# Optimization experiments

Measured on AMD Instinct MI355X. Metric: run time of the kernel, lower is better.

## Reference

```python
import jax, jax.numpy as jnp
import numpy as np

HEAD = 8

def setup_inputs() -> dict:
    key = jax.random.key(0)
    k1, k2 = jax.random.split(key)
    B, S, D = 4, 2048, 512
    x = jax.random.normal(k1, (B, S, D), dtype=jnp.float32)
    Wq = jax.random.normal(k2, (D, D), dtype=jnp.float32) * (1.0 / np.sqrt(D))
    return {"x": x, "Wq": Wq}


def reference(x, Wq):
    # Faithful to source: Q, K, V all use linear_q (bug preserved).
    B, S, D = x.shape
    hd = D // HEAD
    q = jnp.einsum('bsd,de->bse', x, Wq)
    # Q = K = V = q
    qh = q.reshape(B, S, HEAD, hd).transpose(0, 2, 1, 3)  # [B,H,S,hd]
    # scale by sqrt(head_dim): inputs.shape[-1] inside ScaleDotAttentionLayer
    scores = jnp.einsum('bhqd,bhkd->bhqk', qh, qh) / jnp.sqrt(jnp.float32(hd))
    weights = jax.nn.softmax(scores, axis=-1)
    ctx = jnp.einsum('bhqk,bhkd->bhqd', weights, qh)
    out = ctx.transpose(0, 2, 1, 3).reshape(B, S, D)
    return out
```

## Files before the change

### kernel.cpp

```cpp
#include <hip/hip_runtime.h>
#include <hip/hip_fp16.h>
#include <math.h>

#define SS 2048
#define DD 512
#define NH 8
#define HD 64

typedef __attribute__((ext_vector_type(8))) short frag_ab;
typedef __attribute__((ext_vector_type(4))) float frag_cd;

static __device__ inline unsigned int pack_h2(float x, float y) {
    __half2 t = __floats2half2_rn(x, y);
    return *(unsigned int*)&t;
}

__global__ __launch_bounds__(256, 4) void gemm_kernel(const float* __restrict__ x,
                                                      const float* __restrict__ w,
                                                      unsigned short* __restrict__ q) {
    __shared__ __align__(16) unsigned short Ah[2][64 * 72];
    __shared__ __align__(16) unsigned short Bt[2][64 * 72];
    const int tid = threadIdx.x;
    const int lane = tid & 63, wv = tid >> 6;
    const int a = lane & 15, g = lane >> 4;
    const int bm = blockIdx.x, bn = blockIdx.y;

    frag_cd acc[4] = {};
    const int asr = tid >> 4;
    const int ac4 = (tid & 15) * 4;
    const int bnn = (tid & 31) * 2;
    const int bkk = (tid >> 5) * 8;

    float4 av[4];
    float2 bv[8];
    #pragma unroll
    for (int p = 0; p < 4; ++p)
        av[p] = *(const float4*)(x + (size_t)(bm * 64 + asr + p * 16) * 512 + ac4);
    #pragma unroll
    for (int j = 0; j < 8; ++j)
        bv[j] = *(const float2*)(w + (size_t)(bkk + j) * 512 + bn * 64 + bnn);

    for (int it = 0; it < 8; ++it) {
        const int cur = it & 1;
        #pragma unroll
        for (int p = 0; p < 4; ++p) {
            uint2 hh = { pack_h2(av[p].x, av[p].y), pack_h2(av[p].z, av[p].w) };
            *(uint2*)&Ah[cur][(asr + p * 16) * 72 + ac4] = hh;
        }
        {
            unsigned int t0[4], t1[4];
            #pragma unroll
            for (int j = 0; j < 4; ++j) {
                t0[j] = pack_h2(bv[2 * j].x, bv[2 * j + 1].x);
                t1[j] = pack_h2(bv[2 * j].y, bv[2 * j + 1].y);
            }
            *(uint4*)&Bt[cur][bnn * 72 + bkk]       = *(uint4*)t0;
            *(uint4*)&Bt[cur][(bnn + 1) * 72 + bkk] = *(uint4*)t1;
        }
        __syncthreads();
        if (it < 7) {
            const int k0 = (it + 1) * 64;
            #pragma unroll
            for (int p = 0; p < 4; ++p)
                av[p] = *(const float4*)(x + (size_t)(bm * 64 + asr + p * 16) * 512 + k0 + ac4);
            #pragma unroll
            for (int j = 0; j < 8; ++j)
                bv[j] = *(const float2*)(w + (size_t)(k0 + bkk + j) * 512 + bn * 64 + bnn);
        }
        #pragma unroll
        for (int kh = 0; kh < 2; ++kh) {
            const frag_ab bf = *(const frag_ab*)&Bt[cur][(wv * 16 + a) * 72 + kh * 32 + g * 8];
            #pragma unroll
            for (int mt = 0; mt < 4; ++mt) {
                const frag_ab af = *(const frag_ab*)&Ah[cur][(mt * 16 + a) * 72 + kh * 32 + g * 8];
                acc[mt] = __builtin_amdgcn_mfma_f32_16x16x32_f16(af, bf, acc[mt], 0, 0, 0);
            }
        }
    }
    #pragma unroll
    for (int mt = 0; mt < 4; ++mt)
        #pragma unroll
        for (int r = 0; r < 4; ++r) {
            const int m = bm * 64 + mt * 16 + g * 4 + r;
            const int n = bn * 64 + wv * 16 + a;
            __half hv = __float2half_rn(acc[mt][r]);
            q[(size_t)m * 512 + n] = *(unsigned short*)&hv;
        }
}

__global__ __launch_bounds__(512, 4) void attn_kernel(const __half* __restrict__ qg,
                                                      float* __restrict__ out) {
    __shared__ __align__(16) unsigned short Kt[2][64 * 72];
    __shared__ __align__(16) unsigned short Vt[2][64 * 64];
    __shared__ __align__(16) unsigned short Pq[8][32 * 72];

    const int tid = threadIdx.x;
    const int lane = tid & 63, wv = tid >> 6;
    const int a = lane & 15, g = lane >> 4;
    const int a7 = a & 7;
    const int qq = wv & 3;
    const int kv = wv >> 2;
    const int bid = blockIdx.x;
    const int qt = bid & 15;
    const int h  = (bid >> 4) & 7;
    const int b  = bid >> 7;

    const unsigned short* qbh = (const unsigned short*)qg + (size_t)b * SS * DD + h * HD;
    const int qrow0 = qt * 128 + qq * 32;

    frag_ab qf[2][2];
    const __half2 qsc = __float2half2_rn(0.18033688011112042f);
    #pragma unroll
    for (int nt = 0; nt < 2; ++nt)
        #pragma unroll
        for (int kh = 0; kh < 2; ++kh) {
            frag_ab t = *(const frag_ab*)(qbh + (size_t)(qrow0 + nt * 16 + a) * DD + kh * 32 + g * 8);
            __half2* ph = (__half2*)&t;
            #pragma unroll
            for (int i = 0; i < 4; ++i) ph[i] = __hmul2(ph[i], qsc);
            qf[nt][kh] = t;
        }

    frag_cd oacc[4][2] = {};
    float lsum[2] = {0.f, 0.f};

    const int t8 = tid & 255;
    const int f0 = (t8 & 31) * 2;
    const int u8 = t8 >> 5;
    const int r0 = u8 * 8;
    const int keybase = (tid >> 8) * 1024;
    unsigned short* Ks = Kt[tid >> 8];
    unsigned short* Vs = Vt[tid >> 8];
    unsigned short* myP = Pq[wv];

    unsigned int d[8];
    #pragma unroll
    for (int k = 0; k < 8; ++k)
        d[k] = *(const unsigned int*)(qbh + (size_t)(keybase + r0 + k) * DD + f0);

    const unsigned short* Kc = Kt[kv];
    const unsigned short* Vc = Vt[kv];
    const float coff = -11.541560327111707f;

    for (int it = 0; it < 16; ++it) {
        __syncthreads();
        #pragma unroll
        for (int k = 0; k < 8; ++k)
            *(unsigned int*)&Ks[(r0 + k) * 72 + f0] = d[k];
        {
            unsigned int vlo[4], vhi[4];
            #pragma unroll
            for (int j = 0; j < 4; ++j) {
                vlo[j] = (d[2 * j] & 0xFFFFu) | (d[2 * j + 1] << 16);
                vhi[j] = (d[2 * j] >> 16)     | (d[2 * j + 1] & 0xFFFF0000u);
            }
            *(uint4*)&Vs[f0 * 64 + ((u8 ^ (f0 & 7)) << 3)]             = *(uint4*)vlo;
            *(uint4*)&Vs[(f0 + 1) * 64 + ((u8 ^ ((f0 + 1) & 7)) << 3)] = *(uint4*)vhi;
        }
        __syncthreads();

        if (it + 1 < 16) {
            const int kb = keybase + (it + 1) * 64;
            #pragma unroll
            for (int k = 0; k < 8; ++k)
                d[k] = *(const unsigned int*)(qbh + (size_t)(kb + r0 + k) * DD + f0);
        }

        #pragma unroll
        for (int kt = 0; kt < 4; ++kt) {
            const frag_ab ka0 = *(const frag_ab*)&Kc[(kt * 16 + a) * 72 + g * 8];
            const frag_ab ka1 = *(const frag_ab*)&Kc[(kt * 16 + a) * 72 + 32 + g * 8];
            #pragma unroll
            for (int nt = 0; nt < 2; ++nt) {
                frag_cd c = {coff, coff, coff, coff};
                c = __builtin_amdgcn_mfma_f32_16x16x32_f16(ka0, qf[nt][0], c, 0, 0, 0);
                c = __builtin_amdgcn_mfma_f32_16x16x32_f16(ka1, qf[nt][1], c, 0, 0, 0);
                const float p0 = __builtin_amdgcn_exp2f(c[0]);
                const float p1 = __builtin_amdgcn_exp2f(c[1]);
                const float p2 = __builtin_amdgcn_exp2f(c[2]);
                const float p3 = __builtin_amdgcn_exp2f(c[3]);
                lsum[nt] += (p0 + p1) + (p2 + p3);
                uint2 pw = { pack_h2(p0, p1), pack_h2(p2, p3) };
                *(uint2*)&myP[(nt * 16 + a) * 72 + kt * 16 + g * 4] = pw;
            }
        }
        #pragma unroll
        for (int kh = 0; kh < 2; ++kh) {
            frag_ab va[4], pb[2];
            #pragma unroll
            for (int ft = 0; ft < 4; ++ft)
                va[ft] = *(const frag_ab*)&Vc[(ft * 16 + a) * 64 + (((4 * kh + g) ^ a7) << 3)];
            #pragma unroll
            for (int nt = 0; nt < 2; ++nt)
                pb[nt] = *(const frag_ab*)&myP[(nt * 16 + a) * 72 + kh * 32 + g * 8];
            #pragma unroll
            for (int ft = 0; ft < 4; ++ft)
                #pragma unroll
                for (int nt = 0; nt < 2; ++nt)
                    oacc[ft][nt] = __builtin_amdgcn_mfma_f32_16x16x32_f16(va[ft], pb[nt], oacc[ft][nt], 0, 0, 0);
        }
    }

    #pragma unroll
    for (int nt = 0; nt < 2; ++nt) {
        lsum[nt] += __shfl_xor(lsum[nt], 16, 64);
        lsum[nt] += __shfl_xor(lsum[nt], 32, 64);
    }
    __syncthreads();
    float* Obuf = (float*)&Pq[0][0];
    float* Lbuf = (float*)&Kt[0][0];
    if (kv == 1) {
        #pragma unroll
        for (int ft = 0; ft < 4; ++ft)
            #pragma unroll
            for (int nt = 0; nt < 2; ++nt)
                #pragma unroll
                for (int r = 0; r < 4; ++r)
                    Obuf[qq * 2112 + (ft * 16 + g * 4 + r) * 33 + nt * 16 + a] = oacc[ft][nt][r];
        if (g == 0)
            #pragma unroll
            for (int nt = 0; nt < 2; ++nt)
                Lbuf[qq * 32 + nt * 16 + a] = lsum[nt];
    }
    __syncthreads();
    if (kv == 0) {
        #pragma unroll
        for (int nt = 0; nt < 2; ++nt) {
            const float inv = 1.f / (lsum[nt] + Lbuf[qq * 32 + nt * 16 + a]);
            float* op = out + ((size_t)b * SS + qrow0 + nt * 16 + a) * DD + h * HD;
            #pragma unroll
            for (int ft = 0; ft < 4; ++ft) {
                const int fb = ft * 16 + g * 4;
                float4 vv = {
                    (oacc[ft][nt][0] + Obuf[qq * 2112 + (fb + 0) * 33 + nt * 16 + a]) * inv,
                    (oacc[ft][nt][1] + Obuf[qq * 2112 + (fb + 1) * 33 + nt * 16 + a]) * inv,
                    (oacc[ft][nt][2] + Obuf[qq * 2112 + (fb + 2) * 33 + nt * 16 + a]) * inv,
                    (oacc[ft][nt][3] + Obuf[qq * 2112 + (fb + 3) * 33 + nt * 16 + a]) * inv };
                *(float4*)(op + fb) = vv;
            }
        }
    }
}

extern "C" void kernel_launch(void* const* d_in, const int* in_sizes, int n_in,
                              void* d_out, int out_size, void* d_ws, size_t ws_size,
                              hipStream_t stream) {
    const float* x  = (const float*)d_in[0];
    const float* wq = (const float*)d_in[1];
    float* out = (float*)d_out;
    unsigned short* q_h = (unsigned short*)d_ws;

    dim3 ggrid(128, 8);
    gemm_kernel<<<ggrid, 256, 0, stream>>>(x, wq, q_h);
    attn_kernel<<<512, 512, 0, stream>>>((const __half*)q_h, out);
}
```

Baseline: 127.9 us.

## Keep softmax probabilities in registers via lane shuffles and halve query tile per block

The attention kernel no longer stages the P matrix through shared memory. Cross-lane shuffles rearrange the exp'd score fragments from the QK^T MFMA output layout into the B-operand layout for the PV MFMA. Each wave now handles 16 query rows instead of 32, the grid doubles to 1024 blocks, launch bounds request 8 blocks per SM, and the V swizzle is changed to match. This removes the LDS round trip and shrinks shared memory so occupancy can rise, at the cost of loading K/V tiles twice as often per query row and extra shuffle instructions.

```diff
diff --git a/kernel.cpp b/kernel.cpp
--- a/kernel.cpp
+++ b/kernel.cpp
@@ -88,41 +88,37 @@
         }
 }
 
-__global__ __launch_bounds__(512, 4) void attn_kernel(const __half* __restrict__ qg,
+__global__ __launch_bounds__(512, 8) void attn_kernel(const __half* __restrict__ qg,
                                                       float* __restrict__ out) {
     __shared__ __align__(16) unsigned short Kt[2][64 * 72];
     __shared__ __align__(16) unsigned short Vt[2][64 * 64];
-    __shared__ __align__(16) unsigned short Pq[8][32 * 72];
 
     const int tid = threadIdx.x;
     const int lane = tid & 63, wv = tid >> 6;
     const int a = lane & 15, g = lane >> 4;
-    const int a7 = a & 7;
     const int qq = wv & 3;
     const int kv = wv >> 2;
     const int bid = blockIdx.x;
-    const int qt = bid & 15;
-    const int h  = (bid >> 4) & 7;
-    const int b  = bid >> 7;
+    const int qt = bid & 31;
+    const int h  = (bid >> 5) & 7;
+    const int b  = bid >> 8;
 
     const unsigned short* qbh = (const unsigned short*)qg + (size_t)b * SS * DD + h * HD;
-    const int qrow0 = qt * 128 + qq * 32;
-
-    frag_ab qf[2][2];
+    const int qrow0 = qt * 64 + qq * 16;
+
+    frag_ab qf[2];
     const __half2 qsc = __float2half2_rn(0.18033688011112042f);
     #pragma unroll
-    for (int nt = 0; nt < 2; ++nt)
-        #pragma unroll
-        for (int kh = 0; kh < 2; ++kh) {
-            frag_ab t = *(const frag_ab*)(qbh + (size_t)(qrow0 + nt * 16 + a) * DD + kh * 32 + g * 8);
-            __half2* ph = (__half2*)&t;
-            #pragma unroll
-            for (int i = 0; i < 4; ++i) ph[i] = __hmul2(ph[i], qsc);
-            qf[nt][kh] = t;
-        }
-
-    frag_cd oacc[4][2] = {};
-    float lsum[2] = {0.f, 0.f};
+    for (int kh = 0; kh < 2; ++kh) {
+        frag_ab t = *(const frag_ab*)(qbh + (size_t)(qrow0 + a) * DD + kh * 32 + g * 8);
+        __half2* phh = (__half2*)&t;
+        #pragma unroll
+        for (int i = 0; i < 4; ++i) phh[i] = __hmul2(phh[i], qsc);
+        qf[kh] = t;
+    }
+
+    frag_cd oacc[4] = {};
+    float lsum = 0.f;
 
     const int t8 = tid & 255;
     const int f0 = (t8 & 31) * 2;
@@ -131,7 +127,7 @@
     const int keybase = (tid >> 8) * 1024;
     unsigned short* Ks = Kt[tid >> 8];
     unsigned short* Vs = Vt[tid >> 8];
-    unsigned short* myP = Pq[wv];
+    const int vsw = (u8 ^ (t8 & 7)) << 3;
 
     unsigned int d[8];
     #pragma unroll
@@ -141,6 +137,8 @@
     const unsigned short* Kc = Kt[kv];
     const unsigned short* Vc = Vt[kv];
     const float coff = -11.541560327111707f;
+    const bool hi32 = (lane & 32) != 0;
+    const bool hi16 = (lane & 16) != 0;
 
     for (int it = 0; it < 16; ++it) {
         __syncthreads();
@@ -154,8 +152,8 @@
                 vlo[j] = (d[2 * j] & 0xFFFFu) | (d[2 * j + 1] << 16);
                 vhi[j] = (d[2 * j] >> 16)     | (d[2 * j + 1] & 0xFFFF0000u);
             }
-            *(uint4*)&Vs[f0 * 64 + ((u8 ^ (f0 & 7)) << 3)]             = *(uint4*)vlo;
-            *(uint4*)&Vs[(f0 + 1) * 64 + ((u8 ^ ((f0 + 1) & 7)) << 3)] = *(uint4*)vhi;
+            *(uint4*)&Vs[f0 * 64 + vsw]       = *(uint4*)vlo;
+            *(uint4*)&Vs[(f0 + 1) * 64 + vsw] = *(uint4*)vhi;
         }
         __syncthreads();
 
@@ -166,78 +164,84 @@
                 d[k] = *(const unsigned int*)(qbh + (size_t)(kb + r0 + k) * DD + f0);
         }
 
+        unsigned int ph[4][2];
         #pragma unroll
         for (int kt = 0; kt < 4; ++kt) {
             const frag_ab ka0 = *(const frag_ab*)&Kc[(kt * 16 + a) * 72 + g * 8];
             const frag_ab ka1 = *(const frag_ab*)&Kc[(kt * 16 + a) * 72 + 32 + g * 8];
-            #pragma unroll
-            for (int nt = 0; nt < 2; ++nt) {
-                frag_cd c = {coff, coff, coff, coff};
-                c = __builtin_amdgcn_mfma_f32_16x16x32_f16(ka0, qf[nt][0], c, 0, 0, 0);
-                c = __builtin_amdgcn_mfma_f32_16x16x32_f16(ka1, qf[nt][1], c, 0, 0, 0);
-                const float p0 = __builtin_amdgcn_exp2f(c[0]);
-                const float p1 = __builtin_amdgcn_exp2f(c[1]);
-                const float p2 = __builtin_amdgcn_exp2f(c[2]);
-                const float p3 = __builtin_amdgcn_exp2f(c[3]);
-                lsum[nt] += (p0 + p1) + (p2 + p3);
-                uint2 pw = { pack_h2(p0, p1), pack_h2(p2, p3) };
-                *(uint2*)&myP[(nt * 16 + a) * 72 + kt * 16 + g * 4] = pw;
-            }
+            frag_cd c = {coff, coff, coff, coff};
+            c = __builtin_amdgcn_mfma_f32_16x16x32_f16(ka0, qf[0], c, 0, 0, 0);
+            c = __builtin_amdgcn_mfma_f32_16x16x32_f16(ka1, qf[1], c, 0, 0, 0);
+            const float p0 = __builtin_amdgcn_exp2f(c[0]);
+            const float p1 = __builtin_amdgcn_exp2f(c[1]);
+            const float p2 = __builtin_amdgcn_exp2f(c[2]);
+            const float p3 = __builtin_amdgcn_exp2f(c[3]);
+            lsum += (p0 + p1) + (p2 + p3);
+            ph[kt][0] = pack_h2(p0, p1);
+            ph[kt][1] = pack_h2(p2, p3);
+        }
+        #pragma unroll
+        for (int w = 0; w < 2; ++w) {
+            unsigned int s01 = hi32 ? ph[0][w] : ph[1][w];
+            unsigned int t01 = __shfl_xor(s01, 32, 64);
+            ph[0][w] = hi32 ? t01 : ph[0][w];
+            ph[1][w] = hi32 ? ph[1][w] : t01;
+            unsigned int s23 = hi32 ? ph[2][w] : ph[3][w];
+            unsigned int t23 = __shfl_xor(s23, 32, 64);
+            ph[2][w] = hi32 ? t23 : ph[2][w];
+            ph[3][w] = hi32 ? ph[3][w] : t23;
+        }
+        #pragma unroll
+        for (int w = 0; w < 2; ++w) {
+            unsigned int s01 = hi16 ? ph[0][w] : ph[1][w];
+            unsigned int t01 = __shfl_xor(s01, 16, 64);
+            ph[0][w] = hi16 ? t01 : ph[0][w];
+            ph[1][w] = hi16 ? ph[1][w] : t01;
+            unsigned int s23 = hi16 ? ph[2][w] : ph[3][w];
+            unsigned int t23 = __shfl_xor(s23, 16, 64);
+            ph[2][w] = hi16 ? t23 : ph[2][w];
+            ph[3][w] = hi16 ? ph[3][w] : t23;
         }
         #pragma unroll
         for (int kh = 0; kh < 2; ++kh) {
-            frag_ab va[4], pb[2];
-            #pragma unroll
-            for (int ft = 0; ft < 4; ++ft)
-                va[ft] = *(const frag_ab*)&Vc[(ft * 16 + a) * 64 + (((4 * kh + g) ^ a7) << 3)];
-            #pragma unroll
-            for (int nt = 0; nt < 2; ++nt)
-                pb[nt] = *(const frag_ab*)&myP[(nt * 16 + a) * 72 + kh * 32 + g * 8];
-            #pragma unroll
-            for (int ft = 0; ft < 4; ++ft)
-                #pragma unroll
-                for (int nt = 0; nt < 2; ++nt)
-                    oacc[ft][nt] = __builtin_amdgcn_mfma_f32_16x16x32_f16(va[ft], pb[nt], oacc[ft][nt], 0, 0, 0);
-        }
-    }
-
-    #pragma unroll
-    for (int nt = 0; nt < 2; ++nt) {
-        lsum[nt] += __shfl_xor(lsum[nt], 16, 64);
-        lsum[nt] += __shfl_xor(lsum[nt], 32, 64);
-    }
+            __attribute__((aligned(16))) unsigned int pw4[4] =
+                { ph[2 * kh][0], ph[2 * kh][1], ph[2 * kh + 1][0], ph[2 * kh + 1][1] };
+            const frag_ab pb = *(const frag_ab*)pw4;
+            #pragma unroll
+            for (int ft = 0; ft < 4; ++ft) {
+                const frag_ab va = *(const frag_ab*)
+                    &Vc[(ft * 16 + a) * 64 + (((4 * kh + g) ^ ((a >> 1) & 7)) << 3)];
+                oacc[ft] = __builtin_amdgcn_mfma_f32_16x16x32_f16(va, pb, oacc[ft], 0, 0, 0);
+            }
+        }
+    }
+
+    lsum += __shfl_xor(lsum, 16, 64);
+    lsum += __shfl_xor(lsum, 32, 64);
     __syncthreads();
-    float* Obuf = (float*)&Pq[0][0];
-    float* Lbuf = (float*)&Kt[0][0];
+    float* Obuf = (float*)&Kt[0][0];
+    float* Lbuf = (float*)&Vt[0][0];
     if (kv == 1) {
         #pragma unroll
         for (int ft = 0; ft < 4; ++ft)
             #pragma unroll
-            for (int nt = 0; nt < 2; ++nt)
-                #pragma unroll
-                for (int r = 0; r < 4; ++r)
-                    Obuf[qq * 2112 + (ft * 16 + g * 4 + r) * 33 + nt * 16 + a] = oacc[ft][nt][r];
-        if (g == 0)
-            #pragma unroll
-            for (int nt = 0; nt < 2; ++nt)
-                Lbuf[qq * 32 + nt * 16 + a] = lsum[nt];
+            for (int r = 0; r < 4; ++r)
+                Obuf[qq * 1088 + (ft * 16 + g * 4 + r) * 17 + a] = oacc[ft][r];
+        if (g == 0) Lbuf[qq * 16 + a] = lsum;
     }
     __syncthreads();
     if (kv == 0) {
-        #pragma unroll
-        for (int nt = 0; nt < 2; ++nt) {
-            const float inv = 1.f / (lsum[nt] + Lbuf[qq * 32 + nt * 16 + a]);
-            float* op = out + ((size_t)b * SS + qrow0 + nt * 16 + a) * DD + h * HD;
-            #pragma unroll
-            for (int ft = 0; ft < 4; ++ft) {
-                const int fb = ft * 16 + g * 4;
-                float4 vv = {
-                    (oacc[ft][nt][0] + Obuf[qq * 2112 + (fb + 0) * 33 + nt * 16 + a]) * inv,
-                    (oacc[ft][nt][1] + Obuf[qq * 2112 + (fb + 1) * 33 + nt * 16 + a]) * inv,
-                    (oacc[ft][nt][2] + Obuf[qq * 2112 + (fb + 2) * 33 + nt * 16 + a]) * inv,
-                    (oacc[ft][nt][3] + Obuf[qq * 2112 + (fb + 3) * 33 + nt * 16 + a]) * inv };
-                *(float4*)(op + fb) = vv;
-            }
+        const float inv = 1.f / (lsum + Lbuf[qq * 16 + a]);
+        float* op = out + ((size_t)b * SS + qrow0 + a) * DD + h * HD;
+        #pragma unroll
+        for (int ft = 0; ft < 4; ++ft) {
+            const int fb = ft * 16 + g * 4;
+            float4 vv = {
+                (oacc[ft][0] + Obuf[qq * 1088 + (fb + 0) * 17 + a]) * inv,
+                (oacc[ft][1] + Obuf[qq * 1088 + (fb + 1) * 17 + a]) * inv,
+                (oacc[ft][2] + Obuf[qq * 1088 + (fb + 2) * 17 + a]) * inv,
+                (oacc[ft][3] + Obuf[qq * 1088 + (fb + 3) * 17 + a]) * inv };
+            *(float4*)(op + fb) = vv;
         }
     }
 }
@@ -252,5 +256,5 @@
 
     dim3 ggrid(128, 8);
     gemm_kernel<<<ggrid, 256, 0, stream>>>(x, wq, q_h);
-    attn_kernel<<<512, 512, 0, stream>>>((const __half*)q_h, out);
-}
+    attn_kernel<<<1024, 512, 0, stream>>>((const __half*)q_h, out);
+}
```

Result: slower. 144.1 us (+12.7%).

## Keep softmax probabilities in registers via lane shuffles instead of LDS round-trip

Applied to the files above, without the earlier changes.

Removes the per-wave P staging buffer in shared memory. The fp16-packed probabilities are now transposed between MFMA output and input layouts with two stages of cross-lane xor shuffles, and the V swizzle pattern is changed to match. Shared memory is collapsed into one byte array, which lowers LDS use per block and may allow more blocks per CU. The cost is extra shuffle and select instructions and more register pressure in the inner loop.

```diff
diff --git a/kernel.cpp b/kernel.cpp
--- a/kernel.cpp
+++ b/kernel.cpp
@@ -90,14 +90,13 @@
 
 __global__ __launch_bounds__(512, 4) void attn_kernel(const __half* __restrict__ qg,
                                                       float* __restrict__ out) {
-    __shared__ __align__(16) unsigned short Kt[2][64 * 72];
-    __shared__ __align__(16) unsigned short Vt[2][64 * 64];
-    __shared__ __align__(16) unsigned short Pq[8][32 * 72];
+    __shared__ __align__(16) unsigned char LDSB[34816];
+    unsigned short* KtB = (unsigned short*)LDSB;
+    unsigned short* VtB = (unsigned short*)(LDSB + 18432);
 
     const int tid = threadIdx.x;
     const int lane = tid & 63, wv = tid >> 6;
     const int a = lane & 15, g = lane >> 4;
-    const int a7 = a & 7;
     const int qq = wv & 3;
     const int kv = wv >> 2;
     const int bid = blockIdx.x;
@@ -115,9 +114,9 @@
         #pragma unroll
         for (int kh = 0; kh < 2; ++kh) {
             frag_ab t = *(const frag_ab*)(qbh + (size_t)(qrow0 + nt * 16 + a) * DD + kh * 32 + g * 8);
-            __half2* ph = (__half2*)&t;
-            #pragma unroll
-            for (int i = 0; i < 4; ++i) ph[i] = __hmul2(ph[i], qsc);
+            __half2* phh = (__half2*)&t;
+            #pragma unroll
+            for (int i = 0; i < 4; ++i) phh[i] = __hmul2(phh[i], qsc);
             qf[nt][kh] = t;
         }
 
@@ -129,18 +128,20 @@
     const int u8 = t8 >> 5;
     const int r0 = u8 * 8;
     const int keybase = (tid >> 8) * 1024;
-    unsigned short* Ks = Kt[tid >> 8];
-    unsigned short* Vs = Vt[tid >> 8];
-    unsigned short* myP = Pq[wv];
+    unsigned short* Ks = KtB + (tid >> 8) * 4608;
+    unsigned short* Vs = VtB + (tid >> 8) * 4096;
+    const int vsw = (u8 ^ (t8 & 7)) << 3;
 
     unsigned int d[8];
     #pragma unroll
     for (int k = 0; k < 8; ++k)
         d[k] = *(const unsigned int*)(qbh + (size_t)(keybase + r0 + k) * DD + f0);
 
-    const unsigned short* Kc = Kt[kv];
-    const unsigned short* Vc = Vt[kv];
+    const unsigned short* Kc = KtB + kv * 4608;
+    const unsigned short* Vc = VtB + kv * 4096;
     const float coff = -11.541560327111707f;
+    const bool hi32 = (lane & 32) != 0;
+    const bool hi16 = (lane & 16) != 0;
 
     for (int it = 0; it < 16; ++it) {
         __syncthreads();
@@ -154,8 +155,8 @@
                 vlo[j] = (d[2 * j] & 0xFFFFu) | (d[2 * j + 1] << 16);
                 vhi[j] = (d[2 * j] >> 16)     | (d[2 * j + 1] & 0xFFFF0000u);
             }
-            *(uint4*)&Vs[f0 * 64 + ((u8 ^ (f0 & 7)) << 3)]             = *(uint4*)vlo;
-            *(uint4*)&Vs[(f0 + 1) * 64 + ((u8 ^ ((f0 + 1) & 7)) << 3)] = *(uint4*)vhi;
+            *(uint4*)&Vs[f0 * 64 + vsw]       = *(uint4*)vlo;
+            *(uint4*)&Vs[(f0 + 1) * 64 + vsw] = *(uint4*)vhi;
         }
         __syncthreads();
 
@@ -166,6 +167,7 @@
                 d[k] = *(const unsigned int*)(qbh + (size_t)(kb + r0 + k) * DD + f0);
         }
 
+        unsigned int ph[2][4][2];
         #pragma unroll
         for (int kt = 0; kt < 4; ++kt) {
             const frag_ab ka0 = *(const frag_ab*)&Kc[(kt * 16 + a) * 72 + g * 8];
@@ -180,24 +182,52 @@
                 const float p2 = __builtin_amdgcn_exp2f(c[2]);
                 const float p3 = __builtin_amdgcn_exp2f(c[3]);
                 lsum[nt] += (p0 + p1) + (p2 + p3);
-                uint2 pw = { pack_h2(p0, p1), pack_h2(p2, p3) };
-                *(uint2*)&myP[(nt * 16 + a) * 72 + kt * 16 + g * 4] = pw;
+                ph[nt][kt][0] = pack_h2(p0, p1);
+                ph[nt][kt][1] = pack_h2(p2, p3);
+            }
+        }
+        #pragma unroll
+        for (int nt = 0; nt < 2; ++nt) {
+            #pragma unroll
+            for (int w = 0; w < 2; ++w) {
+                unsigned int s01 = hi32 ? ph[nt][0][w] : ph[nt][1][w];
+                unsigned int t01 = __shfl_xor(s01, 32, 64);
+                ph[nt][0][w] = hi32 ? t01 : ph[nt][0][w];
+                ph[nt][1][w] = hi32 ? ph[nt][1][w] : t01;
+                unsigned int s23 = hi32 ? ph[nt][2][w] : ph[nt][3][w];
+                unsigned int t23 = __shfl_xor(s23, 32, 64);
+                ph[nt][2][w] = hi32 ? t23 : ph[nt][2][w];
+                ph[nt][3][w] = hi32 ? ph[nt][3][w] : t23;
+            }
+            #pragma unroll
+            for (int w = 0; w < 2; ++w) {
+                unsigned int s01 = hi16 ? ph[nt][0][w] : ph[nt][1][w];
+                unsigned int t01 = __shfl_xor(s01, 16, 64);
+                ph[nt][0][w] = hi16 ? t01 : ph[nt][0][w];
+                ph[nt][1][w] = hi16 ? ph[nt][1][w] : t01;
+                unsigned int s23 = hi16 ? ph[nt][2][w] : ph[nt][3][w];
+                unsigned int t23 = __shfl_xor(s23, 16, 64);
+                ph[nt][2][w] = hi16 ? t23 : ph[nt][2][w];
+                ph[nt][3][w] = hi16 ? ph[nt][3][w] : t23;
             }
         }
         #pragma unroll
         for (int kh = 0; kh < 2; ++kh) {
-            frag_ab va[4], pb[2];
+            frag_ab va[4];
             #pragma unroll
             for (int ft = 0; ft < 4; ++ft)
-                va[ft] = *(const frag_ab*)&Vc[(ft * 16 + a) * 64 + (((4 * kh + g) ^ a7) << 3)];
-            #pragma unroll
-            for (int nt = 0; nt < 2; ++nt)
-                pb[nt] = *(const frag_ab*)&myP[(nt * 16 + a) * 72 + kh * 32 + g * 8];
-            #pragma unroll
-            for (int ft = 0; ft < 4; ++ft)
+                va[ft] = *(const frag_ab*)
+                    &Vc[(ft * 16 + a) * 64 + (((4 * kh + g) ^ ((a >> 1) & 7)) << 3)];
+            #pragma unroll
+            for (int nt = 0; nt < 2; ++nt) {
+                __attribute__((aligned(16))) unsigned int pw4[4] =
+                    { ph[nt][2 * kh][0], ph[nt][2 * kh][1],
+                      ph[nt][2 * kh + 1][0], ph[nt][2 * kh + 1][1] };
+                const frag_ab pb = *(const frag_ab*)pw4;
                 #pragma unroll
-                for (int nt = 0; nt < 2; ++nt)
-                    oacc[ft][nt] = __builtin_amdgcn_mfma_f32_16x16x32_f16(va[ft], pb[nt], oacc[ft][nt], 0, 0, 0);
+                for (int ft = 0; ft < 4; ++ft)
+                    oacc[ft][nt] = __builtin_amdgcn_mfma_f32_16x16x32_f16(va[ft], pb, oacc[ft][nt], 0, 0, 0);
+            }
         }
     }
 
@@ -207,8 +237,8 @@
         lsum[nt] += __shfl_xor(lsum[nt], 32, 64);
     }
     __syncthreads();
-    float* Obuf = (float*)&Pq[0][0];
-    float* Lbuf = (float*)&Kt[0][0];
+    float* Obuf = (float*)LDSB;
+    float* Lbuf = (float*)(LDSB + 33792);
     if (kv == 1) {
         #pragma unroll
         for (int ft = 0; ft < 4; ++ft)
```

Result: no change. 128.6 us (+0.6%).

## Feed softmax probabilities to PV MFMA straight from registers, dropping P LDS staging

Applied to the files above, without the earlier changes.

Instead of writing the exp'd probabilities to a per-wave LDS buffer and reading them back as 16x16x32 operands, each QK^T output fragment is packed into fp16 registers and used directly as the B operand of 16x16x16 MFMAs against V. The V swizzle is changed to match the new 4-element read pattern, and LDS is consolidated into one shared byte array, shrinking it by removing the P buffer. This removes LDS round-trips and the associated latency for P, and may raise occupancy, at the cost of using twice as many smaller-K MFMA instructions for the PV product.

```diff
diff --git a/kernel.cpp b/kernel.cpp
--- a/kernel.cpp
+++ b/kernel.cpp
@@ -9,6 +9,7 @@
 
 typedef __attribute__((ext_vector_type(8))) short frag_ab;
 typedef __attribute__((ext_vector_type(4))) float frag_cd;
+typedef __attribute__((ext_vector_type(4))) _Float16 frag_b4;
 
 static __device__ inline unsigned int pack_h2(float x, float y) {
     __half2 t = __floats2half2_rn(x, y);
@@ -90,14 +91,13 @@
 
 __global__ __launch_bounds__(512, 4) void attn_kernel(const __half* __restrict__ qg,
                                                       float* __restrict__ out) {
-    __shared__ __align__(16) unsigned short Kt[2][64 * 72];
-    __shared__ __align__(16) unsigned short Vt[2][64 * 64];
-    __shared__ __align__(16) unsigned short Pq[8][32 * 72];
+    __shared__ __align__(16) unsigned char LDSB[34816];
+    unsigned short* KtB = (unsigned short*)LDSB;
+    unsigned short* VtB = (unsigned short*)(LDSB + 18432);
 
     const int tid = threadIdx.x;
     const int lane = tid & 63, wv = tid >> 6;
     const int a = lane & 15, g = lane >> 4;
-    const int a7 = a & 7;
     const int qq = wv & 3;
     const int kv = wv >> 2;
     const int bid = blockIdx.x;
@@ -115,9 +115,9 @@
         #pragma unroll
         for (int kh = 0; kh < 2; ++kh) {
             frag_ab t = *(const frag_ab*)(qbh + (size_t)(qrow0 + nt * 16 + a) * DD + kh * 32 + g * 8);
-            __half2* ph = (__half2*)&t;
-            #pragma unroll
-            for (int i = 0; i < 4; ++i) ph[i] = __hmul2(ph[i], qsc);
+            __half2* phh = (__half2*)&t;
+            #pragma unroll
+            for (int i = 0; i < 4; ++i) phh[i] = __hmul2(phh[i], qsc);
             qf[nt][kh] = t;
         }
 
@@ -129,18 +129,19 @@
     const int u8 = t8 >> 5;
     const int r0 = u8 * 8;
     const int keybase = (tid >> 8) * 1024;
-    unsigned short* Ks = Kt[tid >> 8];
-    unsigned short* Vs = Vt[tid >> 8];
-    unsigned short* myP = Pq[wv];
+    unsigned short* Ks = KtB + (tid >> 8) * 4608;
+    unsigned short* Vs = VtB + (tid >> 8) * 4096;
+    const int vsw = (u8 ^ (t8 & 7)) << 3;
 
     unsigned int d[8];
     #pragma unroll
     for (int k = 0; k < 8; ++k)
         d[k] = *(const unsigned int*)(qbh + (size_t)(keybase + r0 + k) * DD + f0);
 
-    const unsigned short* Kc = Kt[kv];
-    const unsigned short* Vc = Vt[kv];
+    const unsigned short* Kc = KtB + kv * 4608;
+    const unsigned short* Vc = VtB + kv * 4096;
     const float coff = -11.541560327111707f;
+    const int sv = (a >> 1) & 7;
 
     for (int it = 0; it < 16; ++it) {
         __syncthreads();
@@ -154,8 +155,8 @@
                 vlo[j] = (d[2 * j] & 0xFFFFu) | (d[2 * j + 1] << 16);
                 vhi[j] = (d[2 * j] >> 16)     | (d[2 * j + 1] & 0xFFFF0000u);
             }
-            *(uint4*)&Vs[f0 * 64 + ((u8 ^ (f0 & 7)) << 3)]             = *(uint4*)vlo;
-            *(uint4*)&Vs[(f0 + 1) * 64 + ((u8 ^ ((f0 + 1) & 7)) << 3)] = *(uint4*)vhi;
+            *(uint4*)&Vs[f0 * 64 + vsw]       = *(uint4*)vlo;
+            *(uint4*)&Vs[(f0 + 1) * 64 + vsw] = *(uint4*)vhi;
         }
         __syncthreads();
 
@@ -170,6 +171,7 @@
         for (int kt = 0; kt < 4; ++kt) {
             const frag_ab ka0 = *(const frag_ab*)&Kc[(kt * 16 + a) * 72 + g * 8];
             const frag_ab ka1 = *(const frag_ab*)&Kc[(kt * 16 + a) * 72 + 32 + g * 8];
+            frag_b4 pbk[2];
             #pragma unroll
             for (int nt = 0; nt < 2; ++nt) {
                 frag_cd c = {coff, coff, coff, coff};
@@ -180,24 +182,19 @@
                 const float p2 = __builtin_amdgcn_exp2f(c[2]);
                 const float p3 = __builtin_amdgcn_exp2f(c[3]);
                 lsum[nt] += (p0 + p1) + (p2 + p3);
-                uint2 pw = { pack_h2(p0, p1), pack_h2(p2, p3) };
-                *(uint2*)&myP[(nt * 16 + a) * 72 + kt * 16 + g * 4] = pw;
-            }
-        }
-        #pragma unroll
-        for (int kh = 0; kh < 2; ++kh) {
-            frag_ab va[4], pb[2];
-            #pragma unroll
-            for (int ft = 0; ft < 4; ++ft)
-                va[ft] = *(const frag_ab*)&Vc[(ft * 16 + a) * 64 + (((4 * kh + g) ^ a7) << 3)];
-            #pragma unroll
-            for (int nt = 0; nt < 2; ++nt)
-                pb[nt] = *(const frag_ab*)&myP[(nt * 16 + a) * 72 + kh * 32 + g * 8];
-            #pragma unroll
-            for (int ft = 0; ft < 4; ++ft)
-                #pragma unroll
-                for (int nt = 0; nt < 2; ++nt)
-                    oacc[ft][nt] = __builtin_amdgcn_mfma_f32_16x16x32_f16(va[ft], pb[nt], oacc[ft][nt], 0, 0, 0);
+                union { unsigned int u[2]; frag_b4 h; } pu;
+                pu.u[0] = pack_h2(p0, p1);
+                pu.u[1] = pack_h2(p2, p3);
+                pbk[nt] = pu.h;
+            }
+            const int vch = ((2 * kt + (g >> 1)) ^ sv) << 3;
+            const int vof = (g & 1) << 2;
+            #pragma unroll
+            for (int ft = 0; ft < 4; ++ft) {
+                const frag_b4 va = *(const frag_b4*)&Vc[(ft * 16 + a) * 64 + vch + vof];
+                oacc[ft][0] = __builtin_amdgcn_mfma_f32_16x16x16f16(va, pbk[0], oacc[ft][0], 0, 0, 0);
+                oacc[ft][1] = __builtin_amdgcn_mfma_f32_16x16x16f16(va, pbk[1], oacc[ft][1], 0, 0, 0);
+            }
         }
     }
 
@@ -207,8 +204,8 @@
         lsum[nt] += __shfl_xor(lsum[nt], 32, 64);
     }
     __syncthreads();
-    float* Obuf = (float*)&Pq[0][0];
-    float* Lbuf = (float*)&Kt[0][0];
+    float* Obuf = (float*)LDSB;
+    float* Lbuf = (float*)(LDSB + 33792);
     if (kv == 1) {
         #pragma unroll
         for (int ft = 0; ft < 4; ++ft)
```

After: 126.5 us. No clear change (-1.1%).
